# Optimization experiments

Hardware: AMD Instinct MI355X
Metric: run time of the kernel (lower is better)

Reference implementation:

```python
import jax, jax.numpy as jnp
import numpy as np

B, L, H, E = 8, 1024, 8, 64
S, D = 1024, 64


def fp(x):
    # power-norm with p=2: norm(x) * x^2 / norm(x^2)
    norm = jnp.sqrt(jnp.sum(x * x, axis=-1, keepdims=True))
    px = x * x  # x^p, p=2
    pnorm = jnp.sqrt(jnp.sum(px * px, axis=-1, keepdims=True))
    return norm * px / pnorm


def phi_p(x):
    return fp(jax.nn.relu(x))


def setup_inputs() -> dict:
    key = jax.random.key(0)
    kq, kk, kv = jax.random.split(key, 3)
    queries = jax.random.normal(kq, (B, L, H, E), dtype=jnp.float32)
    keys = jax.random.normal(kk, (B, S, H, E), dtype=jnp.float32)
    values = jax.random.normal(kv, (B, S, H, D), dtype=jnp.float32)
    # all-False mask: masked_fill(-inf) + fp() would NaN otherwise (see notes)
    attn_mask = jnp.zeros((B, 1, L, S), dtype=bool)
    return {"queries": queries, "keys": keys, "values": values, "attn_mask": attn_mask}


def reference(queries, keys, values, attn_mask):
    qt = phi_p(queries)              # [B,L,H,E]
    kt = phi_p(keys)                 # [B,S,H,E]
    scores = jnp.einsum('blhe,bshe->bhls', qt, kt)  # [B,H,L,S]
    scores = jnp.where(attn_mask, -jnp.inf, scores)  # mask_flag=True path
    # NB: original computes scale = 1/sqrt(E) but never applies it.
    A = jax.nn.softmax(fp(scores), axis=-1)  # dropout is identity at eval
    V = jnp.einsum('bhls,bshd->blhd', A, values)  # [B,L,H,D]
    return V
```

## Files before the change

kernel.cpp:

```cpp
#include <hip/hip_runtime.h>
#include <hip/hip_bf16.h>


#define B_ 8
#define L_ 1024
#define H_ 8
#define E_ 64
#define S_ 1024
#define D_ 64
#define BH_ 64

typedef _Float16 f16_t;
typedef _Float16 f16x8 __attribute__((ext_vector_type(8)));
typedef _Float16 f16x4v __attribute__((ext_vector_type(4)));
typedef float f32x4 __attribute__((ext_vector_type(4)));
typedef unsigned u32x4 __attribute__((ext_vector_type(4)));

#define MFMA16F(a, b, c) __builtin_amdgcn_mfma_f32_16x16x32_f16(a, b, c, 0, 0, 0)
#define GLDS16(g, l)                                                        \
  __builtin_amdgcn_global_load_lds(                                         \
      (const __attribute__((address_space(1))) void*)(g),                   \
      (__attribute__((address_space(3))) void*)(l), 16, 0, 0)

#if __has_builtin(__builtin_amdgcn_exp2f)
#define EXP2(x) __builtin_amdgcn_exp2f(x)
#else
#define EXP2(x) exp2f(x)
#endif

static __device__ __forceinline__ unsigned pkh(float a, float b) {
  return __builtin_bit_cast(unsigned, __builtin_amdgcn_cvt_pkrtz(a, b));
}

static __device__ __forceinline__ void pl32_swap(unsigned& x, unsigned& y) {
#if __has_builtin(__builtin_amdgcn_permlane32_swap)
  auto r = __builtin_amdgcn_permlane32_swap(x, y, false, false);
  x = r[0];
  y = r[1];
#else
  unsigned xs = __shfl_xor((int)x, 32, 64), ys = __shfl_xor((int)y, 32, 64);
  bool hi = (threadIdx.x & 32) != 0;
  unsigned nx = hi ? ys : x;
  unsigned ny = hi ? y : xs;
  x = nx;
  y = ny;
#endif
}

static __device__ __forceinline__ void pl16_swap(unsigned& x, unsigned& y) {
#if __has_builtin(__builtin_amdgcn_permlane16_swap)
  auto r = __builtin_amdgcn_permlane16_swap(x, y, false, false);
  x = r[0];
  y = r[1];
#else
  unsigned xs = __shfl_xor((int)x, 16, 64), ys = __shfl_xor((int)y, 16, 64);
  bool odd = (threadIdx.x & 16) != 0;
  unsigned nx = odd ? ys : x;
  unsigned ny = odd ? y : xs;
  x = nx;
  y = ny;
#endif
}

__global__ __launch_bounds__(256) void prep_kernel(
    const float* __restrict__ q, const float* __restrict__ k,
    const float* __restrict__ v, f16_t* __restrict__ qf,
    f16_t* __restrict__ kf, f16_t* __restrict__ vt) {
  __shared__ float tile[32][68];
  int bid = blockIdx.x;
  if (bid < 8192) {
    int row = bid * 16 + (threadIdx.x >> 4);
    int p = threadIdx.x & 15;
    const float* src;
    f16_t* dst;
    int r = row;
    if (r < B_ * L_ * H_) { src = q; dst = qf; }
    else { r -= B_ * L_ * H_; src = k; dst = kf; }
    int b = r >> 13;
    int l = (r >> 3) & 1023;
    int h = r & 7;
    float4 x = ((const float4*)(src + (size_t)r * 64))[p];
    float s0 = fmaxf(x.x, 0.f) * fmaxf(x.x, 0.f);
    float s1 = fmaxf(x.y, 0.f) * fmaxf(x.y, 0.f);
    float s2 = fmaxf(x.z, 0.f) * fmaxf(x.z, 0.f);
    float s3 = fmaxf(x.w, 0.f) * fmaxf(x.w, 0.f);
    float sum2 = (s0 + s1) + (s2 + s3);
    float sum4 = fmaf(s0, s0, s1 * s1) + fmaf(s2, s2, s3 * s3);
#pragma unroll
    for (int off = 1; off < 16; off <<= 1) {
      sum2 += __shfl_xor(sum2, off, 64);
      sum4 += __shfl_xor(sum4, off, 64);
    }
    float sc = (sum4 > 0.f) ? sqrtf(sum2 / sum4) : 0.f;
    f16x4v o = {(f16_t)(sc * s0), (f16_t)(sc * s1), (f16_t)(sc * s2),
                (f16_t)(sc * s3)};
    int c = p >> 1, e = (p & 1) * 4;
    int col = (((c ^ (l & 7)) << 3) | e);
    *(f16x4v*)(dst + ((size_t)(b * H_ + h) * 1024 + l) * 64 + col) = o;
  } else {
    int vb = bid - 8192;
    int bh = vb >> 5;
    int st = vb & 31;
    int b = bh >> 3, h = bh & 7;
    int t = threadIdx.x;
    int sl = t >> 3, dp = t & 7;
    const float* src =
        v + (((size_t)(b * S_ + st * 32 + sl) * H_ + h) * D_) + dp * 8;
    float4 f0 = ((const float4*)src)[0];
    float4 f1 = ((const float4*)src)[1];
    *(float4*)&tile[sl][dp * 8] = f0;
    *(float4*)&tile[sl][dp * 8 + 4] = f1;
    __syncthreads();
    int d = t >> 2, sc = t & 3;
    f16_t tmp[8];
#pragma unroll
    for (int j = 0; j < 8; ++j) tmp[j] = (f16_t)tile[sc * 8 + j][d];
    f16_t* dst = vt + (((size_t)bh * 32 + st) * 64 + d) * 32 + sc * 8;
    *(uint4*)dst = *(const uint4*)tmp;
  }
}

__global__ __launch_bounds__(256, 4) void attn_kernel(
    const f16_t* __restrict__ qf, const f16_t* __restrict__ kf,
    const f16_t* __restrict__ vt, float* __restrict__ out) {
  __shared__ __align__(16) f16_t k_t[2][2048];
  __shared__ __align__(16) f16_t v_t[2][2048];

  int bh = blockIdx.x & 63;
  int qb = blockIdx.x >> 6;
  int b = bh >> 3, h = bh & 7;
  int tid = threadIdx.x;
  int wave = tid >> 6, lane = tid & 63;
  int g = lane >> 4, n = lane & 15;

  const f16_t* qf_b = qf + ((size_t)bh * L_ + qb * 64) * 64;
  const f16_t* kf_b = kf + (size_t)bh * S_ * 64;
  const f16_t* vt_b = vt + (size_t)bh * 32 * 2048;

  int arow = wave * 16 + n;
  int qoff = arow * 64 + ((g ^ (n & 7)) << 3);
  f16x8 qa0 = *(const f16x8*)(qf_b + qoff);
  f16x8 qa1 = *(const f16x8*)(qf_b + (qoff ^ 32));

  int koff = n * 64 + ((g ^ (n & 7)) << 3);
  int lds_o = tid * 8;

  const f32x4 fzero = {0.f, 0.f, 0.f, 0.f};
  f32x4 acc2 = fzero, acc4 = fzero, mx = fzero;

  const f16_t* kg = kf_b;
#pragma unroll 2
  for (int t = 0; t < 32; ++t) {
    f16x8 b00 = *(const f16x8*)(kg + koff);
    f16x8 b01 = *(const f16x8*)(kg + (koff ^ 32));
    f16x8 b10 = *(const f16x8*)(kg + koff + 1024);
    f16x8 b11 = *(const f16x8*)(kg + (koff ^ 32) + 1024);
    kg += 2048;
    f32x4 sc0 = MFMA16F(b00, qa0, fzero);
    sc0 = MFMA16F(b01, qa1, sc0);
    f32x4 sc1 = MFMA16F(b10, qa0, fzero);
    sc1 = MFMA16F(b11, qa1, sc1);
    f32x4 t0 = sc0 * sc0, t1 = sc1 * sc1;
    acc2 += t0 + t1;
    acc4 += t0 * t0;
    acc4 += t1 * t1;
    mx = __builtin_elementwise_max(mx, __builtin_elementwise_max(t0, t1));
  }
  float a2 = (acc2[0] + acc2[1]) + (acc2[2] + acc2[3]);
  float a4 = (acc4[0] + acc4[1]) + (acc4[2] + acc4[3]);
  float m2 = fmaxf(fmaxf(mx[0], mx[1]), fmaxf(mx[2], mx[3]));
  a2 += __shfl_xor(a2, 16, 64);
  a4 += __shfl_xor(a4, 16, 64);
  m2 = fmaxf(m2, __shfl_xor(m2, 16, 64));
  a2 += __shfl_xor(a2, 32, 64);
  a4 += __shfl_xor(a4, 32, 64);
  m2 = fmaxf(m2, __shfl_xor(m2, 32, 64));
  const float LOG2E = 1.44269504f;
  float c2 = (a4 > 0.f) ? (sqrtf(a2 / a4) * LOG2E) : 0.f;
  float cm2 = c2 * m2;

  f32x4 pv[4];
#pragma unroll
  for (int dg = 0; dg < 4; ++dg) pv[dg] = fzero;
  f32x4 denv = fzero;

  GLDS16(kf_b + lds_o, &k_t[0][lds_o]);
  GLDS16(vt_b + lds_o, &v_t[0][lds_o]);
  for (int t = 0; t < 32; ++t) {
    __syncthreads();
    if (t < 31) {
      int go = (t + 1) * 2048 + lds_o;
      int bs = (t + 1) & 1;
      GLDS16(kf_b + go, &k_t[bs][lds_o]);
      GLDS16(vt_b + go, &v_t[bs][lds_o]);
    }
    const f16_t* kt = k_t[t & 1];
    const f16_t* vl = v_t[t & 1];
    f16x8 vb[4];
#pragma unroll
    for (int dg = 0; dg < 4; ++dg)
      vb[dg] = *(const f16x8*)(vl + n * 32 + dg * 512 + g * 8);
    f16x8 b00 = *(const f16x8*)(kt + koff);
    f16x8 b01 = *(const f16x8*)(kt + (koff ^ 32));
    f16x8 b10 = *(const f16x8*)(kt + koff + 1024);
    f16x8 b11 = *(const f16x8*)(kt + (koff ^ 32) + 1024);
    f32x4 sc0 = MFMA16F(b00, qa0, fzero);
    sc0 = MFMA16F(b01, qa1, sc0);
    f32x4 sc1 = MFMA16F(b10, qa0, fzero);
    sc1 = MFMA16F(b11, qa1, sc1);
    f32x4 e0 = sc0 * sc0 * c2 - cm2;
    f32x4 e1 = sc1 * sc1 * c2 - cm2;
    f32x4 w0, w1;
#pragma unroll
    for (int r = 0; r < 4; ++r) { w0[r] = EXP2(e0[r]); w1[r] = EXP2(e1[r]); }
    denv += w0 + w1;
    unsigned X0 = pkh(w0[0], w0[1]), X1 = pkh(w0[2], w0[3]);
    unsigned Y0 = pkh(w1[0], w1[1]), Y1 = pkh(w1[2], w1[3]);
    pl32_swap(X0, Y0);
    pl16_swap(X0, Y0);
    pl32_swap(X1, Y1);
    pl16_swap(X1, Y1);
    u32x4 fu = {X0, X1, Y0, Y1};
    f16x8 wa = __builtin_bit_cast(f16x8, fu);
#pragma unroll
    for (int dg = 0; dg < 4; ++dg) pv[dg] = MFMA16F(wa, vb[dg], pv[dg]);
  }
  float den = (denv[0] + denv[1]) + (denv[2] + denv[3]);
  den += __shfl_xor(den, 16, 64);
  den += __shfl_xor(den, 32, 64);
#pragma unroll
  for (int r = 0; r < 4; ++r) {
    float dr = __shfl(den, g * 4 + r, 64);
    float inv = 1.f / dr;
    int l = qb * 64 + wave * 16 + g * 4 + r;
    float* op = out + (((size_t)b * L_ + l) * H_ + h) * D_;
#pragma unroll
    for (int dg = 0; dg < 4; ++dg) op[dg * 16 + n] = pv[dg][r] * inv;
  }
}

extern "C" void kernel_launch(void* const* d_in, const int* in_sizes, int n_in,
                              void* d_out, int out_size, void* d_ws, size_t ws_size,
                              hipStream_t stream) {
  const float* q = (const float*)d_in[0];
  const float* k = (const float*)d_in[1];
  const float* v = (const float*)d_in[2];
  float* out = (float*)d_out;

  const size_t NE = (size_t)B_ * L_ * H_ * E_;
  f16_t* qf = (f16_t*)d_ws;
  f16_t* kf = qf + NE;
  f16_t* vt = kf + NE;

  prep_kernel<<<8192 + 2048, 256, 0, stream>>>(q, k, v, qf, kf, vt);
  attn_kernel<<<BH_ * (L_ / 64), 256, 0, stream>>>(qf, kf, vt, out);
}
```

Baseline: 157.3 us.

## Process two query tiles per wave and stage K through LDS in stats pass

```diff
diff --git a/kernel.cpp b/kernel.cpp
--- a/kernel.cpp
+++ b/kernel.cpp
@@ -120,7 +120,7 @@
   }
 }
 
-__global__ __launch_bounds__(256, 4) void attn_kernel(
+__global__ __launch_bounds__(256, 2) void attn_kernel(
     const f16_t* __restrict__ qf, const f16_t* __restrict__ kf,
     const f16_t* __restrict__ vt, float* __restrict__ out) {
   __shared__ __align__(16) f16_t k_t[2][2048];
@@ -133,59 +133,91 @@
   int wave = tid >> 6, lane = tid & 63;
   int g = lane >> 4, n = lane & 15;
 
-  const f16_t* qf_b = qf + ((size_t)bh * L_ + qb * 64) * 64;
+  const f16_t* qf_b = qf + ((size_t)bh * L_ + qb * 128) * 64;
   const f16_t* kf_b = kf + (size_t)bh * S_ * 64;
   const f16_t* vt_b = vt + (size_t)bh * 32 * 2048;
 
-  int arow = wave * 16 + n;
-  int qoff = arow * 64 + ((g ^ (n & 7)) << 3);
-  f16x8 qa0 = *(const f16x8*)(qf_b + qoff);
-  f16x8 qa1 = *(const f16x8*)(qf_b + (qoff ^ 32));
+  int arow = wave * 32 + n;
+  int qoff0 = arow * 64 + ((g ^ (n & 7)) << 3);
+  int qoff1 = qoff0 + 16 * 64;
+  f16x8 qa0_0 = *(const f16x8*)(qf_b + qoff0);
+  f16x8 qa1_0 = *(const f16x8*)(qf_b + (qoff0 ^ 32));
+  f16x8 qa0_1 = *(const f16x8*)(qf_b + qoff1);
+  f16x8 qa1_1 = *(const f16x8*)(qf_b + (qoff1 ^ 32));
 
   int koff = n * 64 + ((g ^ (n & 7)) << 3);
   int lds_o = tid * 8;
 
   const f32x4 fzero = {0.f, 0.f, 0.f, 0.f};
-  f32x4 acc2 = fzero, acc4 = fzero, mx = fzero;
-
-  const f16_t* kg = kf_b;
-#pragma unroll 2
+  f32x4 acc2_0 = fzero, acc4_0 = fzero, mx_0 = fzero;
+  f32x4 acc2_1 = fzero, acc4_1 = fzero, mx_1 = fzero;
+
+  GLDS16(kf_b + lds_o, &k_t[0][lds_o]);
   for (int t = 0; t < 32; ++t) {
-    f16x8 b00 = *(const f16x8*)(kg + koff);
-    f16x8 b01 = *(const f16x8*)(kg + (koff ^ 32));
-    f16x8 b10 = *(const f16x8*)(kg + koff + 1024);
-    f16x8 b11 = *(const f16x8*)(kg + (koff ^ 32) + 1024);
-    kg += 2048;
-    f32x4 sc0 = MFMA16F(b00, qa0, fzero);
-    sc0 = MFMA16F(b01, qa1, sc0);
-    f32x4 sc1 = MFMA16F(b10, qa0, fzero);
-    sc1 = MFMA16F(b11, qa1, sc1);
-    f32x4 t0 = sc0 * sc0, t1 = sc1 * sc1;
-    acc2 += t0 + t1;
-    acc4 += t0 * t0;
-    acc4 += t1 * t1;
-    mx = __builtin_elementwise_max(mx, __builtin_elementwise_max(t0, t1));
-  }
-  float a2 = (acc2[0] + acc2[1]) + (acc2[2] + acc2[3]);
-  float a4 = (acc4[0] + acc4[1]) + (acc4[2] + acc4[3]);
-  float m2 = fmaxf(fmaxf(mx[0], mx[1]), fmaxf(mx[2], mx[3]));
-  a2 += __shfl_xor(a2, 16, 64);
-  a4 += __shfl_xor(a4, 16, 64);
-  m2 = fmaxf(m2, __shfl_xor(m2, 16, 64));
-  a2 += __shfl_xor(a2, 32, 64);
-  a4 += __shfl_xor(a4, 32, 64);
-  m2 = fmaxf(m2, __shfl_xor(m2, 32, 64));
-  const float LOG2E = 1.44269504f;
-  float c2 = (a4 > 0.f) ? (sqrtf(a2 / a4) * LOG2E) : 0.f;
-  float cm2 = c2 * m2;
-
-  f32x4 pv[4];
-#pragma unroll
-  for (int dg = 0; dg < 4; ++dg) pv[dg] = fzero;
-  f32x4 denv = fzero;
-
+    __syncthreads();
+    if (t < 31)
+      GLDS16(kf_b + (t + 1) * 2048 + lds_o, &k_t[(t + 1) & 1][lds_o]);
+    const f16_t* kt = k_t[t & 1];
+    f16x8 b00 = *(const f16x8*)(kt + koff);
+    f16x8 b01 = *(const f16x8*)(kt + (koff ^ 32));
+    f16x8 b10 = *(const f16x8*)(kt + koff + 1024);
+    f16x8 b11 = *(const f16x8*)(kt + (koff ^ 32) + 1024);
+    f32x4 sc0_0 = MFMA16F(b00, qa0_0, fzero);
+    sc0_0 = MFMA16F(b01, qa1_0, sc0_0);
+    f32x4 sc1_0 = MFMA16F(b10, qa0_0, fzero);
+    sc1_0 = MFMA16F(b11, qa1_0, sc1_0);
+    f32x4 sc0_1 = MFMA16F(b00, qa0_1, fzero);
+    sc0_1 = MFMA16F(b01, qa1_1, sc0_1);
+    f32x4 sc1_1 = MFMA16F(b10, qa0_1, fzero);
+    sc1_1 = MFMA16F(b11, qa1_1, sc1_1);
+    f32x4 t0 = sc0_0 * sc0_0, t1 = sc1_0 * sc1_0;
+    acc2_0 += t0 + t1;
+    acc4_0 += t0 * t0;
+    acc4_0 += t1 * t1;
+    mx_0 = __builtin_elementwise_max(mx_0, __builtin_elementwise_max(t0, t1));
+    f32x4 u0 = sc0_1 * sc0_1, u1 = sc1_1 * sc1_1;
+    acc2_1 += u0 + u1;
+    acc4_1 += u0 * u0;
+    acc4_1 += u1 * u1;
+    mx_1 = __builtin_elementwise_max(mx_1, __builtin_elementwise_max(u0, u1));
+  }
   GLDS16(kf_b + lds_o, &k_t[0][lds_o]);
   GLDS16(vt_b + lds_o, &v_t[0][lds_o]);
+
+  const float LOG2E = 1.44269504f;
+  float c2_0, cm2_0, c2_1, cm2_1;
+  {
+    float a2 = (acc2_0[0] + acc2_0[1]) + (acc2_0[2] + acc2_0[3]);
+    float a4 = (acc4_0[0] + acc4_0[1]) + (acc4_0[2] + acc4_0[3]);
+    float m2 = fmaxf(fmaxf(mx_0[0], mx_0[1]), fmaxf(mx_0[2], mx_0[3]));
+    a2 += __shfl_xor(a2, 16, 64);
+    a4 += __shfl_xor(a4, 16, 64);
+    m2 = fmaxf(m2, __shfl_xor(m2, 16, 64));
+    a2 += __shfl_xor(a2, 32, 64);
+    a4 += __shfl_xor(a4, 32, 64);
+    m2 = fmaxf(m2, __shfl_xor(m2, 32, 64));
+    c2_0 = (a4 > 0.f) ? (sqrtf(a2 / a4) * LOG2E) : 0.f;
+    cm2_0 = c2_0 * m2;
+  }
+  {
+    float a2 = (acc2_1[0] + acc2_1[1]) + (acc2_1[2] + acc2_1[3]);
+    float a4 = (acc4_1[0] + acc4_1[1]) + (acc4_1[2] + acc4_1[3]);
+    float m2 = fmaxf(fmaxf(mx_1[0], mx_1[1]), fmaxf(mx_1[2], mx_1[3]));
+    a2 += __shfl_xor(a2, 16, 64);
+    a4 += __shfl_xor(a4, 16, 64);
+    m2 = fmaxf(m2, __shfl_xor(m2, 16, 64));
+    a2 += __shfl_xor(a2, 32, 64);
+    a4 += __shfl_xor(a4, 32, 64);
+    m2 = fmaxf(m2, __shfl_xor(m2, 32, 64));
+    c2_1 = (a4 > 0.f) ? (sqrtf(a2 / a4) * LOG2E) : 0.f;
+    cm2_1 = c2_1 * m2;
+  }
+
+  f32x4 pv0[4], pv1[4];
+#pragma unroll
+  for (int dg = 0; dg < 4; ++dg) { pv0[dg] = fzero; pv1[dg] = fzero; }
+  f32x4 denv0 = fzero, denv1 = fzero;
+
   for (int t = 0; t < 32; ++t) {
     __syncthreads();
     if (t < 31) {
@@ -204,38 +236,69 @@
     f16x8 b01 = *(const f16x8*)(kt + (koff ^ 32));
     f16x8 b10 = *(const f16x8*)(kt + koff + 1024);
     f16x8 b11 = *(const f16x8*)(kt + (koff ^ 32) + 1024);
-    f32x4 sc0 = MFMA16F(b00, qa0, fzero);
-    sc0 = MFMA16F(b01, qa1, sc0);
-    f32x4 sc1 = MFMA16F(b10, qa0, fzero);
-    sc1 = MFMA16F(b11, qa1, sc1);
-    f32x4 e0 = sc0 * sc0 * c2 - cm2;
-    f32x4 e1 = sc1 * sc1 * c2 - cm2;
+    f32x4 sc0_0 = MFMA16F(b00, qa0_0, fzero);
+    sc0_0 = MFMA16F(b01, qa1_0, sc0_0);
+    f32x4 sc1_0 = MFMA16F(b10, qa0_0, fzero);
+    sc1_0 = MFMA16F(b11, qa1_0, sc1_0);
+    f32x4 sc0_1 = MFMA16F(b00, qa0_1, fzero);
+    sc0_1 = MFMA16F(b01, qa1_1, sc0_1);
+    f32x4 sc1_1 = MFMA16F(b10, qa0_1, fzero);
+    sc1_1 = MFMA16F(b11, qa1_1, sc1_1);
+    f32x4 e0 = sc0_0 * sc0_0 * c2_0 - cm2_0;
+    f32x4 e1 = sc1_0 * sc1_0 * c2_0 - cm2_0;
     f32x4 w0, w1;
 #pragma unroll
     for (int r = 0; r < 4; ++r) { w0[r] = EXP2(e0[r]); w1[r] = EXP2(e1[r]); }
-    denv += w0 + w1;
+    denv0 += w0 + w1;
     unsigned X0 = pkh(w0[0], w0[1]), X1 = pkh(w0[2], w0[3]);
     unsigned Y0 = pkh(w1[0], w1[1]), Y1 = pkh(w1[2], w1[3]);
     pl32_swap(X0, Y0);
     pl16_swap(X0, Y0);
     pl32_swap(X1, Y1);
     pl16_swap(X1, Y1);
-    u32x4 fu = {X0, X1, Y0, Y1};
-    f16x8 wa = __builtin_bit_cast(f16x8, fu);
-#pragma unroll
-    for (int dg = 0; dg < 4; ++dg) pv[dg] = MFMA16F(wa, vb[dg], pv[dg]);
-  }
-  float den = (denv[0] + denv[1]) + (denv[2] + denv[3]);
-  den += __shfl_xor(den, 16, 64);
-  den += __shfl_xor(den, 32, 64);
+    u32x4 fu0 = {X0, X1, Y0, Y1};
+    f16x8 wa0 = __builtin_bit_cast(f16x8, fu0);
+    f32x4 f0v = sc0_1 * sc0_1 * c2_1 - cm2_1;
+    f32x4 f1v = sc1_1 * sc1_1 * c2_1 - cm2_1;
+    f32x4 z0, z1;
+#pragma unroll
+    for (int r = 0; r < 4; ++r) { z0[r] = EXP2(f0v[r]); z1[r] = EXP2(f1v[r]); }
+    denv1 += z0 + z1;
+    unsigned P0 = pkh(z0[0], z0[1]), P1 = pkh(z0[2], z0[3]);
+    unsigned Q0 = pkh(z1[0], z1[1]), Q1 = pkh(z1[2], z1[3]);
+    pl32_swap(P0, Q0);
+    pl16_swap(P0, Q0);
+    pl32_swap(P1, Q1);
+    pl16_swap(P1, Q1);
+    u32x4 fu1 = {P0, P1, Q0, Q1};
+    f16x8 wa1 = __builtin_bit_cast(f16x8, fu1);
+#pragma unroll
+    for (int dg = 0; dg < 4; ++dg) {
+      pv0[dg] = MFMA16F(wa0, vb[dg], pv0[dg]);
+      pv1[dg] = MFMA16F(wa1, vb[dg], pv1[dg]);
+    }
+  }
+
+  float den0 = (denv0[0] + denv0[1]) + (denv0[2] + denv0[3]);
+  den0 += __shfl_xor(den0, 16, 64);
+  den0 += __shfl_xor(den0, 32, 64);
+  float den1 = (denv1[0] + denv1[1]) + (denv1[2] + denv1[3]);
+  den1 += __shfl_xor(den1, 16, 64);
+  den1 += __shfl_xor(den1, 32, 64);
 #pragma unroll
   for (int r = 0; r < 4; ++r) {
-    float dr = __shfl(den, g * 4 + r, 64);
-    float inv = 1.f / dr;
-    int l = qb * 64 + wave * 16 + g * 4 + r;
-    float* op = out + (((size_t)b * L_ + l) * H_ + h) * D_;
-#pragma unroll
-    for (int dg = 0; dg < 4; ++dg) op[dg * 16 + n] = pv[dg][r] * inv;
+    float dr0 = __shfl(den0, g * 4 + r, 64);
+    float inv0 = 1.f / dr0;
+    int l0 = qb * 128 + wave * 32 + g * 4 + r;
+    float* op0 = out + (((size_t)b * L_ + l0) * H_ + h) * D_;
+#pragma unroll
+    for (int dg = 0; dg < 4; ++dg) op0[dg * 16 + n] = pv0[dg][r] * inv0;
+    float dr1 = __shfl(den1, g * 4 + r, 64);
+    float inv1 = 1.f / dr1;
+    int l1 = l0 + 16;
+    float* op1 = out + (((size_t)b * L_ + l1) * H_ + h) * D_;
+#pragma unroll
+    for (int dg = 0; dg < 4; ++dg) op1[dg * 16 + n] = pv1[dg][r] * inv1;
   }
 }
 
@@ -253,5 +316,5 @@
   f16_t* vt = kf + NE;
 
   prep_kernel<<<8192 + 2048, 256, 0, stream>>>(q, k, v, qf, kf, vt);
-  attn_kernel<<<BH_ * (L_ / 64), 256, 0, stream>>>(qf, kf, vt, out);
-}
+  attn_kernel<<<BH_ * (L_ / 128), 256, 0, stream>>>(qf, kf, vt, out);
+}
```

Result: no change. 155.0 us (-1.5%).
